# Optimization experiments

Measured on AMD Instinct MI355X. Metric: run time of the kernel, lower is better.

Reference implementation:

```python
import jax, jax.numpy as jnp
import numpy as np

B, T, J, D_IN = 16, 128, 75, 3
HID, OUT, E = 64, 256, 300


def setup_inputs() -> dict:
    key = jax.random.key(0)
    ks = jax.random.split(key, 6)
    x = jax.random.normal(ks[0], (B, T, J, D_IN), dtype=jnp.float32)
    edge_index = jax.random.randint(ks[1], (2, E), 0, J, dtype=jnp.int64)
    W1 = jax.random.normal(ks[2], (D_IN, HID), dtype=jnp.float32) * (1.0 / np.sqrt(D_IN))
    b1 = jax.random.normal(ks[3], (HID,), dtype=jnp.float32) * 0.02
    W2 = jax.random.normal(ks[4], (HID, OUT), dtype=jnp.float32) * (1.0 / np.sqrt(HID))
    b2 = jax.random.normal(ks[5], (OUT,), dtype=jnp.float32) * 0.02
    return {"x": x, "edge_index": edge_index, "W1": W1, "b1": b1, "W2": W2, "b2": b2}


def _gcn_norm(edge_index, num_nodes, dtype):
    # PyG gcn_norm: add self-loops, norm = deg^{-1/2}[src] * deg^{-1/2}[dst]
    loops = jnp.arange(num_nodes, dtype=edge_index.dtype)
    src = jnp.concatenate([edge_index[0], loops])
    dst = jnp.concatenate([edge_index[1], loops])
    deg = jnp.zeros((num_nodes,), dtype).at[dst].add(jnp.ones_like(dst, dtype))
    dis = jax.lax.rsqrt(deg)  # deg >= 1 due to self loops
    norm = dis[src] * dis[dst]  # (E+J,)
    return src, dst, norm


def _gcn_layer(h, W, b, src, dst, norm):
    # h: (BT, J, Din) -> (BT, J, Dout). Linear first, then normalized scatter-add.
    h = h @ W
    msgs = h[:, src, :] * norm[None, :, None]        # (BT, E+J, Dout)
    agg = jnp.zeros_like(h).at[:, dst, :].add(msgs)  # (BT, J, Dout)
    return agg + b


def reference(x, edge_index, W1, b1, W2, b2):
    Bx, Tx, Jx, Dx = x.shape
    h = x.reshape(Bx * Tx, Jx, Dx)
    src, dst, norm = _gcn_norm(edge_index, Jx, x.dtype)
    h = jax.nn.gelu(_gcn_layer(h, W1, b1, src, dst, norm), approximate=False)
    h = jax.nn.gelu(_gcn_layer(h, W2, b2, src, dst, norm), approximate=False)
    return h.reshape(Bx, Tx, Jx, -1)
```

## Files before the change

### kernel.cpp

```cpp
#include <hip/hip_runtime.h>
#include <hip/hip_bf16.h>
#include <math.h>

#define J 75
#define EDGES 300
#define MAXE (EDGES + J)
#define HID 64
#define OUTF 256
#define BT 2048
#define CSTR 68
#define MROWS 80

typedef __attribute__((ext_vector_type(8))) short short8;
typedef __attribute__((ext_vector_type(4))) float f32x4;

__device__ __forceinline__ unsigned short f32_to_bf16_rn(float f) {
    unsigned u = __float_as_uint(f);
    unsigned r = u + 0x7FFFu + ((u >> 16) & 1u);
    return (unsigned short)(r >> 16);
}
__device__ __forceinline__ float bf16_to_f32(unsigned short h) {
    return __uint_as_float(((unsigned)h) << 16);
}
__device__ __forceinline__ float gelu_exact(float v) {
    return 0.5f * v * (1.0f + erff(v * 0.70710678118654752f));
}

__global__ void build_csr_kernel(const int* __restrict__ ei,
                                 int* __restrict__ csr_off,
                                 int* __restrict__ csr_src,
                                 float* __restrict__ csr_norm) {
    __shared__ int   deg[J];
    __shared__ int   off[J + 1];
    __shared__ int   cur[J];
    __shared__ float dis[J];
    const int tid = threadIdx.x;

    if (tid < J) { deg[tid] = 1; cur[tid] = 0; }
    __syncthreads();
    for (int e = tid; e < EDGES; e += blockDim.x)
        atomicAdd(&deg[ei[EDGES + e]], 1);
    __syncthreads();
    if (tid == 0) {
        int s = 0;
        for (int j = 0; j < J; ++j) { off[j] = s; s += deg[j]; }
        off[J] = s;
    }
    if (tid < J) dis[tid] = rsqrtf((float)deg[tid]);
    __syncthreads();
    for (int e = tid; e < EDGES; e += blockDim.x) {
        int s = ei[e], d = ei[EDGES + e];
        int p = off[d] + atomicAdd(&cur[d], 1);
        csr_src[p]  = s;
        csr_norm[p] = dis[s] * dis[d];
    }
    for (int j = tid; j < J; j += blockDim.x) {
        int p = off[j] + atomicAdd(&cur[j], 1);
        csr_src[p]  = j;
        csr_norm[p] = dis[j] * dis[j];
    }
    __syncthreads();
    for (int j = tid; j <= J; j += blockDim.x) csr_off[j] = off[j];
}

__global__ void repack_w2_kernel(const float* __restrict__ W2,
                                 unsigned short* __restrict__ Whi,
                                 unsigned short* __restrict__ Wlo) {
    int t = blockIdx.x * 256 + threadIdx.x;
    int j    = t & 7;
    int lane = (t >> 3) & 63;
    int nt   = (t >> 9) & 15;
    int kc   = t >> 13;
    int k = kc * 32 + (lane >> 4) * 8 + j;
    int n = nt * 16 + (lane & 15);
    float w = W2[k * OUTF + n];
    unsigned short hi = f32_to_bf16_rn(w);
    float lo = w - bf16_to_f32(hi);
    Whi[t] = hi;
    Wlo[t] = f32_to_bf16_rn(lo);
}

__global__ void __launch_bounds__(256, 2) gcn_fused_kernel(
        const float* __restrict__ xg,
        const float* __restrict__ W1,
        const float* __restrict__ b1,
        const float* __restrict__ b2,
        const int*   __restrict__ csr_off,
        const int*   __restrict__ csr_src,
        const float* __restrict__ csr_norm,
        const unsigned short* __restrict__ Whi,
        const unsigned short* __restrict__ Wlo,
        float* __restrict__ outg) {
    __shared__ float xs[J * 3];
    __shared__ float ax[J * 3];
    __shared__ float Bs[J * HID];
    __shared__ __align__(16) float Cs[MROWS * CSTR];
    __shared__ float W1s[3 * HID];
    __shared__ float b1s[HID];
    __shared__ float b2s[OUTF];
    __shared__ int   offs[J + 1];
    __shared__ int   srcs[MAXE];
    __shared__ float nrms[MAXE];

    const int tid  = threadIdx.x;
    const int bt   = blockIdx.x;
    const int wv   = tid >> 6;
    const int lane = tid & 63;
    const int quad = lane >> 4;
    const int l16  = lane & 15;

    if (tid < J + 1) offs[tid] = csr_off[tid];
    for (int i = tid; i < MAXE; i += 256) { srcs[i] = csr_src[i]; nrms[i] = csr_norm[i]; }
    if (tid < 3 * HID) W1s[tid] = W1[tid];
    if (tid < HID)     b1s[tid] = b1[tid];
    if (tid < OUTF)    b2s[tid] = b2[tid];
    for (int i = tid; i < J * 3; i += 256)
        xs[i] = xg[bt * (J * 3) + i];
    __syncthreads();

    for (int idx = tid; idx < J * 3; idx += 256) {
        int j = idx / 3, d = idx - j * 3;
        float s = 0.f;
        int p0 = offs[j], p1 = offs[j + 1];
        for (int p = p0; p < p1; ++p) s += nrms[p] * xs[srcs[p] * 3 + d];
        ax[idx] = s;
    }
    __syncthreads();

    for (int idx = tid; idx < J * HID; idx += 256) {
        int j = idx >> 6, f = idx & 63;
        float v = ax[j * 3 + 0] * W1s[0 * HID + f]
                + ax[j * 3 + 1] * W1s[1 * HID + f]
                + ax[j * 3 + 2] * W1s[2 * HID + f]
                + b1s[f];
        Bs[idx] = gelu_exact(v);
    }
    __syncthreads();

    for (int idx = tid; idx < J * HID; idx += 256) {
        int j = idx >> 6, f = idx & 63;
        float s = 0.f;
        int p0 = offs[j], p1 = offs[j + 1];
        for (int p = p0; p < p1; ++p) s += nrms[p] * Bs[srcs[p] * HID + f];
        Cs[j * CSTR + f] = s;
    }
    for (int idx = tid; idx < (MROWS - J) * HID; idx += 256) {
        int j = J + (idx >> 6), f = idx & 63;
        Cs[j * CSTR + f] = 0.f;
    }
    __syncthreads();

    f32x4 acc[5][4] = {};
    const short8* Whi8 = (const short8*)Whi;
    const short8* Wlo8 = (const short8*)Wlo;

#pragma unroll
    for (int kc = 0; kc < 2; ++kc) {
        short8 bhi[4], blo[4];
#pragma unroll
        for (int n4 = 0; n4 < 4; ++n4) {
            int nt = wv * 4 + n4;
            int fi = (kc * 16 + nt) * 64 + lane;
            bhi[n4] = Whi8[fi];
            blo[n4] = Wlo8[fi];
        }
#pragma unroll
        for (int mt = 0; mt < 5; ++mt) {
            const float* ar = &Cs[(mt * 16 + l16) * CSTR + kc * 32 + quad * 8];
            f32x4 a0 = *(const f32x4*)ar;
            f32x4 a1 = *(const f32x4*)(ar + 4);
            float av[8] = {a0.x, a0.y, a0.z, a0.w, a1.x, a1.y, a1.z, a1.w};
            short8 ahi, alo;
#pragma unroll
            for (int i = 0; i < 8; ++i) {
                unsigned short h = f32_to_bf16_rn(av[i]);
                ahi[i] = (short)h;
                alo[i] = (short)f32_to_bf16_rn(av[i] - bf16_to_f32(h));
            }
#pragma unroll
            for (int n4 = 0; n4 < 4; ++n4) {
                acc[mt][n4] = __builtin_amdgcn_mfma_f32_16x16x32_bf16(ahi, bhi[n4], acc[mt][n4], 0, 0, 0);
                acc[mt][n4] = __builtin_amdgcn_mfma_f32_16x16x32_bf16(ahi, blo[n4], acc[mt][n4], 0, 0, 0);
                acc[mt][n4] = __builtin_amdgcn_mfma_f32_16x16x32_bf16(alo, bhi[n4], acc[mt][n4], 0, 0, 0);
            }
        }
    }

    float* outb = outg + (size_t)bt * (J * OUTF);
#pragma unroll
    for (int mt = 0; mt < 5; ++mt) {
#pragma unroll
        for (int n4 = 0; n4 < 4; ++n4) {
            int o = wv * 64 + n4 * 16 + l16;
            float bias = b2s[o];
#pragma unroll
            for (int r = 0; r < 4; ++r) {
                int row = mt * 16 + quad * 4 + r;
                if (row < J)
                    outb[row * OUTF + o] = gelu_exact(acc[mt][n4][r] + bias);
            }
        }
    }
}

extern "C" void kernel_launch(void* const* d_in, const int* in_sizes, int n_in,
                              void* d_out, int out_size, void* d_ws, size_t ws_size,
                              hipStream_t stream) {
    const float* x  = (const float*)d_in[0];
    const int*   ei = (const int*)d_in[1];
    const float* W1 = (const float*)d_in[2];
    const float* b1 = (const float*)d_in[3];
    const float* W2 = (const float*)d_in[4];
    const float* b2 = (const float*)d_in[5];
    float* out = (float*)d_out;

    char* ws = (char*)d_ws;
    int*   csr_off  = (int*)ws;
    int*   csr_src  = (int*)(ws + 512);
    float* csr_norm = (float*)(ws + 512 + 2048);
    unsigned short* Whi = (unsigned short*)(ws + 4096);
    unsigned short* Wlo = (unsigned short*)(ws + 4096 + 32768);

    build_csr_kernel<<<1, 256, 0, stream>>>(ei, csr_off, csr_src, csr_norm);
    repack_w2_kernel<<<64, 256, 0, stream>>>(W2, Whi, Wlo);
    gcn_fused_kernel<<<BT, 256, 0, stream>>>(x, W1, b1, b2,
                                             csr_off, csr_src, csr_norm,
                                             Whi, Wlo, out);
}
```

Baseline: 223.8 us.

## Merge prep kernels, pre-split bf16 A operand in LDS, use fast GELU

```diff
diff --git a/kernel.cpp b/kernel.cpp
--- a/kernel.cpp
+++ b/kernel.cpp
@@ -8,8 +8,8 @@
 #define HID 64
 #define OUTF 256
 #define BT 2048
-#define CSTR 68
 #define MROWS 80
+#define CSP 152
 
 typedef __attribute__((ext_vector_type(8))) short short8;
 typedef __attribute__((ext_vector_type(4))) float f32x4;
@@ -22,23 +22,51 @@
 __device__ __forceinline__ float bf16_to_f32(unsigned short h) {
     return __uint_as_float(((unsigned)h) << 16);
 }
-__device__ __forceinline__ float gelu_exact(float v) {
-    return 0.5f * v * (1.0f + erff(v * 0.70710678118654752f));
-}
-
-__global__ void build_csr_kernel(const int* __restrict__ ei,
-                                 int* __restrict__ csr_off,
-                                 int* __restrict__ csr_src,
-                                 float* __restrict__ csr_norm) {
+
+__device__ __forceinline__ float gelu_fast(float v) {
+    float u = 0.70710678118654752f * v;
+    float a = fabsf(u);
+    float t = __builtin_amdgcn_rcpf(fmaf(0.3275911f, a, 1.0f));
+    float p = t * fmaf(t, fmaf(t, fmaf(t, fmaf(t, 1.061405429f, -1.453152027f),
+                                       1.421413741f), -0.284496736f), 0.254829592f);
+    float e = __expf(-a * a);
+    float erfa = fmaf(-p, e, 1.0f);
+    float erfu = copysignf(erfa, u);
+    return 0.5f * v * (1.0f + erfu);
+}
+
+__global__ void prep_kernel(const int* __restrict__ ei,
+                            const float* __restrict__ W2,
+                            int* __restrict__ csr_off,
+                            unsigned short* __restrict__ csr_src,
+                            float* __restrict__ csr_norm,
+                            unsigned short* __restrict__ Whi,
+                            unsigned short* __restrict__ Wlo) {
     __shared__ int   deg[J];
     __shared__ int   off[J + 1];
     __shared__ int   cur[J];
     __shared__ float dis[J];
     const int tid = threadIdx.x;
 
+    if (blockIdx.x < 64) {
+        int t = blockIdx.x * 256 + tid;
+        int j    = t & 7;
+        int lane = (t >> 3) & 63;
+        int nt   = (t >> 9) & 15;
+        int kc   = t >> 13;
+        int k = kc * 32 + (lane >> 4) * 8 + j;
+        int n = nt * 16 + (lane & 15);
+        float w = W2[k * OUTF + n];
+        unsigned short hi = f32_to_bf16_rn(w);
+        float lo = w - bf16_to_f32(hi);
+        Whi[t] = hi;
+        Wlo[t] = f32_to_bf16_rn(lo);
+        return;
+    }
+
     if (tid < J) { deg[tid] = 1; cur[tid] = 0; }
     __syncthreads();
-    for (int e = tid; e < EDGES; e += blockDim.x)
+    for (int e = tid; e < EDGES; e += 256)
         atomicAdd(&deg[ei[EDGES + e]], 1);
     __syncthreads();
     if (tid == 0) {
@@ -48,45 +76,28 @@
     }
     if (tid < J) dis[tid] = rsqrtf((float)deg[tid]);
     __syncthreads();
-    for (int e = tid; e < EDGES; e += blockDim.x) {
+    for (int e = tid; e < EDGES; e += 256) {
         int s = ei[e], d = ei[EDGES + e];
         int p = off[d] + atomicAdd(&cur[d], 1);
-        csr_src[p]  = s;
+        csr_src[p]  = (unsigned short)s;
         csr_norm[p] = dis[s] * dis[d];
     }
-    for (int j = tid; j < J; j += blockDim.x) {
+    for (int j = tid; j < J; j += 256) {
         int p = off[j] + atomicAdd(&cur[j], 1);
-        csr_src[p]  = j;
+        csr_src[p]  = (unsigned short)j;
         csr_norm[p] = dis[j] * dis[j];
     }
     __syncthreads();
-    for (int j = tid; j <= J; j += blockDim.x) csr_off[j] = off[j];
-}
-
-__global__ void repack_w2_kernel(const float* __restrict__ W2,
-                                 unsigned short* __restrict__ Whi,
-                                 unsigned short* __restrict__ Wlo) {
-    int t = blockIdx.x * 256 + threadIdx.x;
-    int j    = t & 7;
-    int lane = (t >> 3) & 63;
-    int nt   = (t >> 9) & 15;
-    int kc   = t >> 13;
-    int k = kc * 32 + (lane >> 4) * 8 + j;
-    int n = nt * 16 + (lane & 15);
-    float w = W2[k * OUTF + n];
-    unsigned short hi = f32_to_bf16_rn(w);
-    float lo = w - bf16_to_f32(hi);
-    Whi[t] = hi;
-    Wlo[t] = f32_to_bf16_rn(lo);
-}
-
-__global__ void __launch_bounds__(256, 2) gcn_fused_kernel(
+    for (int j = tid; j <= J; j += 256) csr_off[j] = off[j];
+}
+
+__global__ void __launch_bounds__(256, 3) gcn_fused_kernel(
         const float* __restrict__ xg,
         const float* __restrict__ W1,
         const float* __restrict__ b1,
         const float* __restrict__ b2,
         const int*   __restrict__ csr_off,
-        const int*   __restrict__ csr_src,
+        const unsigned short* __restrict__ csr_src,
         const float* __restrict__ csr_norm,
         const unsigned short* __restrict__ Whi,
         const unsigned short* __restrict__ Wlo,
@@ -94,12 +105,12 @@
     __shared__ float xs[J * 3];
     __shared__ float ax[J * 3];
     __shared__ float Bs[J * HID];
-    __shared__ __align__(16) float Cs[MROWS * CSTR];
+    __shared__ __align__(16) unsigned short Csp[MROWS * CSP];
     __shared__ float W1s[3 * HID];
     __shared__ float b1s[HID];
     __shared__ float b2s[OUTF];
     __shared__ int   offs[J + 1];
-    __shared__ int   srcs[MAXE];
+    __shared__ unsigned short srcs[MAXE];
     __shared__ float nrms[MAXE];
 
     const int tid  = threadIdx.x;
@@ -133,27 +144,45 @@
                 + ax[j * 3 + 1] * W1s[1 * HID + f]
                 + ax[j * 3 + 2] * W1s[2 * HID + f]
                 + b1s[f];
-        Bs[idx] = gelu_exact(v);
+        Bs[idx] = gelu_fast(v);
     }
     __syncthreads();
 
     for (int idx = tid; idx < J * HID; idx += 256) {
         int j = idx >> 6, f = idx & 63;
-        float s = 0.f;
+        float s = 0.f, s2 = 0.f;
         int p0 = offs[j], p1 = offs[j + 1];
-        for (int p = p0; p < p1; ++p) s += nrms[p] * Bs[srcs[p] * HID + f];
-        Cs[j * CSTR + f] = s;
-    }
-    for (int idx = tid; idx < (MROWS - J) * HID; idx += 256) {
-        int j = J + (idx >> 6), f = idx & 63;
-        Cs[j * CSTR + f] = 0.f;
-    }
-    __syncthreads();
-
-    f32x4 acc[5][4] = {};
+        int p = p0;
+        for (; p + 1 < p1; p += 2) {
+            int a = srcs[p], b = srcs[p + 1];
+            float na = nrms[p], nb = nrms[p + 1];
+            s  += na * Bs[a * HID + f];
+            s2 += nb * Bs[b * HID + f];
+        }
+        if (p < p1) s += nrms[p] * Bs[srcs[p] * HID + f];
+        s += s2;
+        unsigned short hi = f32_to_bf16_rn(s);
+        unsigned short lo = f32_to_bf16_rn(s - bf16_to_f32(hi));
+        Csp[j * CSP + f]      = hi;
+        Csp[j * CSP + 64 + f] = lo;
+    }
+    for (int idx = tid; idx < (MROWS - J) * 128; idx += 256) {
+        int j = J + (idx >> 7), c = idx & 127;
+        Csp[j * CSP + c] = 0;
+    }
+    __syncthreads();
+
+    f32x4 acc[5][4];
+#pragma unroll
+    for (int n4 = 0; n4 < 4; ++n4) {
+        float bv = b2s[wv * 64 + n4 * 16 + l16];
+#pragma unroll
+        for (int mt = 0; mt < 5; ++mt)
+            acc[mt][n4] = (f32x4){bv, bv, bv, bv};
+    }
+
     const short8* Whi8 = (const short8*)Whi;
     const short8* Wlo8 = (const short8*)Wlo;
-
 #pragma unroll
     for (int kc = 0; kc < 2; ++kc) {
         short8 bhi[4], blo[4];
@@ -166,17 +195,9 @@
         }
 #pragma unroll
         for (int mt = 0; mt < 5; ++mt) {
-            const float* ar = &Cs[(mt * 16 + l16) * CSTR + kc * 32 + quad * 8];
-            f32x4 a0 = *(const f32x4*)ar;
-            f32x4 a1 = *(const f32x4*)(ar + 4);
-            float av[8] = {a0.x, a0.y, a0.z, a0.w, a1.x, a1.y, a1.z, a1.w};
-            short8 ahi, alo;
-#pragma unroll
-            for (int i = 0; i < 8; ++i) {
-                unsigned short h = f32_to_bf16_rn(av[i]);
-                ahi[i] = (short)h;
-                alo[i] = (short)f32_to_bf16_rn(av[i] - bf16_to_f32(h));
-            }
+            const unsigned short* ar = &Csp[(mt * 16 + l16) * CSP + kc * 32 + quad * 8];
+            short8 ahi = *(const short8*)ar;
+            short8 alo = *(const short8*)(ar + 64);
 #pragma unroll
             for (int n4 = 0; n4 < 4; ++n4) {
                 acc[mt][n4] = __builtin_amdgcn_mfma_f32_16x16x32_bf16(ahi, bhi[n4], acc[mt][n4], 0, 0, 0);
@@ -192,12 +213,11 @@
 #pragma unroll
         for (int n4 = 0; n4 < 4; ++n4) {
             int o = wv * 64 + n4 * 16 + l16;
-            float bias = b2s[o];
 #pragma unroll
             for (int r = 0; r < 4; ++r) {
                 int row = mt * 16 + quad * 4 + r;
                 if (row < J)
-                    outb[row * OUTF + o] = gelu_exact(acc[mt][n4][r] + bias);
+                    outb[row * OUTF + o] = gelu_fast(acc[mt][n4][r]);
             }
         }
     }
@@ -215,14 +235,13 @@
     float* out = (float*)d_out;
 
     char* ws = (char*)d_ws;
-    int*   csr_off  = (int*)ws;
-    int*   csr_src  = (int*)(ws + 512);
-    float* csr_norm = (float*)(ws + 512 + 2048);
-    unsigned short* Whi = (unsigned short*)(ws + 4096);
-    unsigned short* Wlo = (unsigned short*)(ws + 4096 + 32768);
-
-    build_csr_kernel<<<1, 256, 0, stream>>>(ei, csr_off, csr_src, csr_norm);
-    repack_w2_kernel<<<64, 256, 0, stream>>>(W2, Whi, Wlo);
+    int*            csr_off  = (int*)ws;
+    unsigned short* csr_src  = (unsigned short*)(ws + 512);
+    float*          csr_norm = (float*)(ws + 2048);
+    unsigned short* Whi      = (unsigned short*)(ws + 4096);
+    unsigned short* Wlo      = (unsigned short*)(ws + 4096 + 32768);
+
+    prep_kernel<<<65, 256, 0, stream>>>(ei, W2, csr_off, csr_src, csr_norm, Whi, Wlo);
     gcn_fused_kernel<<<BT, 256, 0, stream>>>(x, W1, b1, b2,
                                              csr_off, csr_src, csr_norm,
                                              Whi, Wlo, out);
```

Measured after the change: 221.3 us. No clear change (-1.1%).
